# Kernel optimization log

Hardware: AMD Instinct MI355X
Metric: run time of the kernel (lower is better)

## Reference

```python
import jax, jax.numpy as jnp
import numpy as np
import math

H = 8
D_MODEL = 512
SEQ = 1024  # afr_reduced_cnn_size -> becomes sequence/channel axis
B = 16
KSIZE = 7
D_K = D_MODEL // H


def setup_inputs() -> dict:
    key = jax.random.key(0)
    ks = jax.random.split(key, 9)
    s = 0.02
    return {
        "query": jax.random.normal(ks[0], (B, SEQ, D_MODEL), jnp.float32),
        "key": jax.random.normal(ks[1], (B, SEQ, D_MODEL), jnp.float32),
        "value": jax.random.normal(ks[2], (B, SEQ, D_MODEL), jnp.float32),
        # causal conv params for K and V projections (convs[1], convs[2]); convs[0] is unused in forward
        "conv_k_w": jax.random.normal(ks[3], (SEQ, SEQ, KSIZE), jnp.float32) * s,
        "conv_k_b": jnp.zeros((SEQ,), jnp.float32),
        "conv_v_w": jax.random.normal(ks[4], (SEQ, SEQ, KSIZE), jnp.float32) * s,
        "conv_v_b": jnp.zeros((SEQ,), jnp.float32),
        # output linear (torch Linear: weight [out, in])
        "lin_w": jax.random.normal(ks[5], (D_MODEL, D_MODEL), jnp.float32) * s,
        "lin_b": jnp.zeros((D_MODEL,), jnp.float32),
    }


def _causal_conv1d(x, w, b):
    # x: [B, C, L]; w: [O, I, K]; left-pad K-1 for causality
    pad = w.shape[-1] - 1
    y = jax.lax.conv_general_dilated(
        x, w, window_strides=(1,), padding=[(pad, 0)],
        dimension_numbers=("NCH", "OIH", "NCH"))
    return y + b[None, :, None]


def reference(query, key, value, conv_k_w, conv_k_b, conv_v_w, conv_v_b, lin_w, lin_b):
    nb = query.shape[0]
    # [B, S, d_model] -> [B, h, N, d_k]
    q = query.reshape(nb, -1, H, D_K).transpose(0, 2, 1, 3)
    k = _causal_conv1d(key, conv_k_w, conv_k_b).reshape(nb, -1, H, D_K).transpose(0, 2, 1, 3)
    v = _causal_conv1d(value, conv_v_w, conv_v_b).reshape(nb, -1, H, D_K).transpose(0, 2, 1, 3)
    scores = jnp.einsum("bhnd,bhmd->bhnm", q, k) / math.sqrt(D_K)
    p_attn = jax.nn.softmax(scores, axis=-1)  # dropout is identity at eval
    x = jnp.einsum("bhnm,bhmd->bhnd", p_attn, v)
    x = x.transpose(0, 2, 1, 3).reshape(nb, -1, H * D_K)
    return x @ lin_w.T + lin_b
```

## Files before the change

### kernel.cpp

```cpp
#include <hip/hip_runtime.h>
#include <hip/hip_bf16.h>

typedef unsigned short u16;
typedef __attribute__((ext_vector_type(8))) __bf16 bf16x8;
typedef __attribute__((ext_vector_type(4))) float f32x4;
typedef __attribute__((ext_vector_type(4))) unsigned short u16x4;

#define DEVI static __device__ __forceinline__

DEVI u16 f2bf(float f) {
    union { float f; unsigned u; } v; v.f = f;
    unsigned r = v.u + 0x7fffu + ((v.u >> 16) & 1u);
    return (u16)(r >> 16);
}

DEVI unsigned cvt_pk_bf16(float lo, float hi) {
    unsigned r;
    asm("v_cvt_pk_bf16_f32 %0, %1, %2" : "=v"(r) : "v"(lo), "v"(hi));
    return r;
}

DEVI void gload16(const u16* g, u16* l) {
    __builtin_amdgcn_global_load_lds(
        (const __attribute__((address_space(1))) void*)g,
        (__attribute__((address_space(3))) void*)l, 16, 0, 0);
}


__global__ void k_cast_scale(const float* __restrict__ src, u16* __restrict__ dst,
                             int n, float scale) {
    int i = (blockIdx.x * blockDim.x + threadIdx.x) * 4;
    if (i >= n) return;
    float4 v = *(const float4*)(src + i);
    u16x4 o = { f2bf(v.x * scale), f2bf(v.y * scale), f2bf(v.z * scale), f2bf(v.w * scale) };
    *(u16x4*)(dst + i) = o;
}

__global__ void k_castW2(const float* __restrict__ wk, const float* __restrict__ wv,
                         u16* __restrict__ wtk, u16* __restrict__ wtv) {
    int oi = blockIdx.x * blockDim.x + threadIdx.x;
    const float* p = (blockIdx.y ? wv : wk) + (size_t)oi * 7;
    u16* wt = blockIdx.y ? wtv : wtk;
#pragma unroll
    for (int t = 0; t < 7; ++t)
        wt[(size_t)t * 1048576 + oi] = f2bf(p[t]);
}

__global__ void k_transpose_pad2(const float* __restrict__ xk, const float* __restrict__ xv,
                                 u16* __restrict__ ok, u16* __restrict__ ov) {
    __shared__ float tile[64][65];
    int z = blockIdx.z;
    bool isV = z >= 16;
    int b = isV ? z - 16 : z;
    const float* x = isV ? xv : xk;
    u16* out = isV ? ov : ok;
    int l0 = blockIdx.x * 64, i0 = blockIdx.y * 64;
    int t = threadIdx.x;
    const float* xb = x + (size_t)b * 1024 * 512;
    u16* ob = out + (size_t)b * 520 * 1024;
    if (blockIdx.x == 0 && t < 96) {
        int pr = t >> 4, pc = (t & 15) * 4;
        u16x4 zz = { 0, 0, 0, 0 };
        *(u16x4*)(ob + (size_t)pr * 1024 + i0 + pc) = zz;
    }
    int tr = t >> 4, tc = (t & 15) * 4;
#pragma unroll
    for (int r = 0; r < 4; ++r) {
        int row = tr + r * 16;
        float4 v = *(const float4*)(xb + (size_t)(i0 + row) * 512 + l0 + tc);
        tile[row][tc + 0] = v.x; tile[row][tc + 1] = v.y;
        tile[row][tc + 2] = v.z; tile[row][tc + 3] = v.w;
    }
    __syncthreads();
#pragma unroll
    for (int r = 0; r < 4; ++r) {
        int lr = tr + r * 16;
        u16x4 o = { f2bf(tile[tc + 0][lr]), f2bf(tile[tc + 1][lr]),
                    f2bf(tile[tc + 2][lr]), f2bf(tile[tc + 3][lr]) };
        *(u16x4*)(ob + (size_t)(l0 + 6 + lr) * 1024 + i0 + tc) = o;
    }
}

__global__ __launch_bounds__(256, 2)
void k_conv128(const u16* __restrict__ WtK, const u16* __restrict__ WtV,
               const u16* __restrict__ XtK, const u16* __restrict__ XtV,
               const float* __restrict__ bK, const float* __restrict__ bV,
               u16* __restrict__ YK, u16* __restrict__ YV) {
    __shared__ __align__(16) u16 As[2][8192];
    __shared__ __align__(16) u16 Bs[16896];
    int id = blockIdx.x;
    int o0 = (id & 7) * 128;
    bool isV = (id >> 3) & 1;
    int inner = id >> 4;
    int b = inner & 15;
    int l0 = (inner >> 4) * 256;
    const u16* Wt = isV ? WtV : WtK;
    const u16* Xb = (isV ? XtV : XtK) + (size_t)b * 520 * 1024;
    int tid = threadIdx.x, lane = tid & 63, wave = tid >> 6;
    int q = lane & 15, g = lane >> 4;
    int wm = wave >> 1, wn = wave & 1;

    int sr = tid >> 3;
    int ss = (tid & 7) ^ (sr & 7);

    auto stageA = [&](int ic, int t, int slot) {
        const u16* a = Wt + ((size_t)t << 20) + (size_t)(o0 + sr) * 1024 + (ic << 6) + ss * 8;
        u16* ad = &As[slot][tid * 8];
#pragma unroll
        for (int l = 0; l < 4; ++l)
            gload16(a + (size_t)(l << 5) * 1024, ad + (l << 11));
    };
    auto stageB = [&](int ic) {
        const u16* bb = Xb + (size_t)(l0 + sr) * 1024 + (ic << 6) + ss * 8;
        u16* bd = &Bs[tid * 8];
#pragma unroll
        for (int l = 0; l < 8; ++l)
            gload16(bb + (size_t)(l << 5) * 1024, bd + (l << 11));
        int sr5 = 256 + (sr & 7);
        gload16(Xb + (size_t)(l0 + sr5) * 1024 + (ic << 6) + ss * 8,
                &Bs[sr5 * 64 + (tid & 7) * 8]);
    };

    f32x4 acc[4][8] = {};

    stageB(0);
    stageA(0, 0, 0);
    stageA(0, 1, 1);
    asm volatile("s_waitcnt vmcnt(4)" ::: "memory");
    __builtin_amdgcn_s_barrier();

    int ic2 = 0, t2 = 2;
    for (int ic = 0; ic < 16; ++ic) {
        for (int t = 0; t < 7; ++t) {
            int s = ic * 7 + t;
            const u16* Asl = As[s & 1];
            bf16x8 af[4][2], bfr[4][2];

#pragma unroll
            for (int mf = 0; mf < 4; ++mf) {
                int r = wm * 64 + mf * 16 + q;
                const u16* base = Asl + r * 64;
#pragma unroll
                for (int kk = 0; kk < 2; ++kk)
                    af[mf][kk] = *(const bf16x8*)(base + (((kk * 4 + g) ^ (r & 7)) << 3));
            }
#pragma unroll
            for (int nf = 0; nf < 4; ++nf) {
                int r = wn * 128 + nf * 16 + q + t;
                const u16* base = Bs + r * 64;
#pragma unroll
                for (int kk = 0; kk < 2; ++kk)
                    bfr[nf][kk] = *(const bf16x8*)(base + (((kk * 4 + g) ^ (r & 7)) << 3));
            }
#pragma unroll
            for (int mf = 0; mf < 4; ++mf)
#pragma unroll
                for (int nf = 0; nf < 4; ++nf)
#pragma unroll
                    for (int kk = 0; kk < 2; ++kk)
                        acc[mf][nf] = __builtin_amdgcn_mfma_f32_16x16x32_bf16(
                            af[mf][kk], bfr[nf][kk], acc[mf][nf], 0, 0, 0);

#pragma unroll
            for (int nf = 0; nf < 4; ++nf) {
                int r = wn * 128 + (4 + nf) * 16 + q + t;
                const u16* base = Bs + r * 64;
#pragma unroll
                for (int kk = 0; kk < 2; ++kk)
                    bfr[nf][kk] = *(const bf16x8*)(base + (((kk * 4 + g) ^ (r & 7)) << 3));
            }
#pragma unroll
            for (int mf = 0; mf < 4; ++mf)
#pragma unroll
                for (int nf = 0; nf < 4; ++nf)
#pragma unroll
                    for (int kk = 0; kk < 2; ++kk)
                        acc[mf][4 + nf] = __builtin_amdgcn_mfma_f32_16x16x32_bf16(
                            af[mf][kk], bfr[nf][kk], acc[mf][4 + nf], 0, 0, 0);

            asm volatile("" ::: "memory");
            __builtin_amdgcn_s_barrier();
            if (s + 2 < 112) {
                if (t == 6) stageB(ic + 1);
                stageA(ic2, t2, s & 1);
                if (++t2 == 7) { t2 = 0; ++ic2; }
                asm volatile("s_waitcnt vmcnt(4)" ::: "memory");
            } else {
                asm volatile("s_waitcnt vmcnt(0)" ::: "memory");
            }
            __builtin_amdgcn_s_barrier();
        }
    }

    const float* bias = isV ? bV : bK;
#pragma unroll
    for (int mf = 0; mf < 4; ++mf) {
        int ro = o0 + wm * 64 + mf * 16 + g * 4;
        float b0 = bias[ro + 0], b1 = bias[ro + 1], b2 = bias[ro + 2], b3 = bias[ro + 3];
#pragma unroll
        for (int nf = 0; nf < 8; ++nf) {
            int co = l0 + wn * 128 + nf * 16 + q;
            f32x4 a = acc[mf][nf];
            if (isV) {
                u16x4 o = { f2bf(a[0] + b0), f2bf(a[1] + b1), f2bf(a[2] + b2), f2bf(a[3] + b3) };
                *(u16x4*)&YV[((size_t)b * 512 + co) * 1024 + ro] = o;
            } else {
                u16* yp = &YK[((size_t)b * 1024 + ro) * 512 + co];
                yp[0]    = f2bf(a[0] + b0);
                yp[512]  = f2bf(a[1] + b1);
                yp[1024] = f2bf(a[2] + b2);
                yp[1536] = f2bf(a[3] + b3);
            }
        }
    }
}

__global__ __launch_bounds__(512, 4)
void k_attn2(const u16* __restrict__ Q, const u16* __restrict__ K,
             const u16* __restrict__ Vt, u16* __restrict__ O) {
    __shared__ __align__(16) u16 Ks[2][64 * 64];
    __shared__ __align__(16) u16 Vs[2][64 * 64];
    int b = blockIdx.z, h = blockIdx.y, q0 = blockIdx.x * 128;
    int tid = threadIdx.x, lane = tid & 63, wave = tid >> 6;
    int g = lane >> 4, q = lane & 15;

    const u16* Kb = K + (size_t)b * 1024 * 512 + h * 64;
    const u16* Vb = Vt + ((size_t)b * 512 + h * 64) * 1024;
    const u16* Qb = Q + ((size_t)b * 1024 + q0 + wave * 16 + q) * 512 + h * 64;

    bf16x8 qf[2];
    qf[0] = *(const bf16x8*)(Qb + g * 8);
    qf[1] = *(const bf16x8*)(Qb + 32 + g * 8);

    int sr = tid >> 3;
    int ss = (tid & 7) ^ (sr & 7);
    const u16* ksrc = Kb + (size_t)sr * 512 + ss * 8;
    const u16* vsrc = Vb + (size_t)sr * 1024 + ss * 8;

    f32x4 o[4] = {};
    float lsum = 0.f;

    gload16(ksrc, &Ks[0][tid * 8]);
    gload16(vsrc, &Vs[0][tid * 8]);
    __syncthreads();

#pragma unroll 2
    for (int t = 0; t < 16; ++t) {
        int buf = t & 1;
        if (t < 15) {
            gload16(ksrc + (size_t)(t + 1) * 64 * 512, &Ks[buf ^ 1][tid * 8]);
            gload16(vsrc + (t + 1) * 64, &Vs[buf ^ 1][tid * 8]);
        }
        f32x4 s[4];
#pragma unroll
        for (int mf = 0; mf < 4; ++mf) {
            int r = 16 * mf + q;
            const u16* base = &Ks[buf][r * 64];
            bf16x8 kf0 = *(const bf16x8*)(base + (((g) ^ (q & 7)) << 3));
            bf16x8 kf1 = *(const bf16x8*)(base + (((4 + g) ^ (q & 7)) << 3));
            f32x4 zz = {};
            zz = __builtin_amdgcn_mfma_f32_16x16x32_bf16(kf0, qf[0], zz, 0, 0, 0);
            s[mf] = __builtin_amdgcn_mfma_f32_16x16x32_bf16(kf1, qf[1], zz, 0, 0, 0);
        }
        unsigned w[4][2];
#pragma unroll
        for (int mf = 0; mf < 4; ++mf) {
            f32x4 p;
#pragma unroll
            for (int j = 0; j < 4; ++j) {
                p[j] = exp2f(s[mf][j]);
                lsum += p[j];
            }
            w[mf][0] = cvt_pk_bf16(p[0], p[1]);
            w[mf][1] = cvt_pk_bf16(p[2], p[3]);
        }
        bool hi = lane >= 32;
        int ia = ((g & 1) << 5) + q;
        int ib = ia + 16;
#pragma unroll
        for (int c = 0; c < 2; ++c) {
            unsigned a0 = __shfl(w[2 * c][0], ia), b0 = __shfl(w[2 * c + 1][0], ia);
            unsigned a1 = __shfl(w[2 * c][1], ia), b1 = __shfl(w[2 * c + 1][1], ia);
            unsigned a2 = __shfl(w[2 * c][0], ib), b2 = __shfl(w[2 * c + 1][0], ib);
            unsigned a3 = __shfl(w[2 * c][1], ib), b3 = __shfl(w[2 * c + 1][1], ib);
            union { unsigned u[4]; bf16x8 v8; } pu;
            pu.u[0] = hi ? b0 : a0;
            pu.u[1] = hi ? b1 : a1;
            pu.u[2] = hi ? b2 : a2;
            pu.u[3] = hi ? b3 : a3;
            bf16x8 pb = pu.v8;
#pragma unroll
            for (int df = 0; df < 4; ++df) {
                int rd = 16 * df + q;
                bf16x8 vf = *(const bf16x8*)(&Vs[buf][rd * 64] + (((c * 4 + g) ^ (q & 7)) << 3));
                o[df] = __builtin_amdgcn_mfma_f32_16x16x32_bf16(vf, pb, o[df], 0, 0, 0);
            }
        }
        __syncthreads();
    }

    lsum += __shfl_xor(lsum, 16);
    lsum += __shfl_xor(lsum, 32);
    float inv = 1.0f / lsum;

    unsigned wo[4][2];
#pragma unroll
    for (int df = 0; df < 4; ++df) {
        f32x4 v = o[df];
        v[0] *= inv; v[1] *= inv; v[2] *= inv; v[3] *= inv;
        wo[df][0] = cvt_pk_bf16(v[0], v[1]);
        wo[df][1] = cvt_pk_bf16(v[2], v[3]);
    }
    bool hi = lane >= 32;
    int ia = ((g & 1) << 5) + q;
    int ib = ia + 16;
    u16* Ob = O + ((size_t)b * 1024 + q0 + wave * 16 + q) * 512 + h * 64;
#pragma unroll
    for (int c = 0; c < 2; ++c) {
        unsigned a0 = __shfl(wo[2 * c][0], ia), b0 = __shfl(wo[2 * c + 1][0], ia);
        unsigned a1 = __shfl(wo[2 * c][1], ia), b1 = __shfl(wo[2 * c + 1][1], ia);
        unsigned a2 = __shfl(wo[2 * c][0], ib), b2 = __shfl(wo[2 * c + 1][0], ib);
        unsigned a3 = __shfl(wo[2 * c][1], ib), b3 = __shfl(wo[2 * c + 1][1], ib);
        int4 st;
        st.x = (int)(hi ? b0 : a0);
        st.y = (int)(hi ? b1 : a1);
        st.z = (int)(hi ? b2 : a2);
        st.w = (int)(hi ? b3 : a3);
        *(int4*)(Ob + c * 32 + g * 8) = st;
    }
}

__global__ __launch_bounds__(256, 2)
void k_gemm_out(const u16* __restrict__ A, const u16* __restrict__ Bt,
                const float* __restrict__ bias, float* __restrict__ C) {
    __shared__ __align__(16) u16 As[128 * 64];
    __shared__ __align__(16) u16 Bs[128 * 64];
    int n0 = blockIdx.x * 128, m0 = blockIdx.y * 128;
    int tid = threadIdx.x, lane = tid & 63, wave = tid >> 6;
    int wr = (wave >> 1) * 64, wc = (wave & 1) * 64;
    f32x4 acc[4][4] = {};

    for (int kk = 0; kk < 8; ++kk) {
        int i0 = kk * 64;
        const u16* asrc = A + (size_t)(m0 + (tid >> 3)) * 512 + i0 + (tid & 7) * 8;
        const u16* bsrc = Bt + (size_t)(n0 + (tid >> 3)) * 512 + i0 + (tid & 7) * 8;
        __syncthreads();
#pragma unroll
        for (int s = 0; s < 4; ++s) {
            gload16(asrc + (size_t)s * 32 * 512, &As[s * 2048 + tid * 8]);
            gload16(bsrc + (size_t)s * 32 * 512, &Bs[s * 2048 + tid * 8]);
        }
        __syncthreads();
#pragma unroll
        for (int ks = 0; ks < 2; ++ks) {
            bf16x8 af[4], bfr[4];
#pragma unroll
            for (int m = 0; m < 4; ++m)
                af[m] = *(const bf16x8*)&As[(wr + m * 16 + (lane & 15)) * 64 + ks * 32 + (lane >> 4) * 8];
#pragma unroll
            for (int n = 0; n < 4; ++n)
                bfr[n] = *(const bf16x8*)&Bs[(wc + n * 16 + (lane & 15)) * 64 + ks * 32 + (lane >> 4) * 8];
#pragma unroll
            for (int m = 0; m < 4; ++m)
#pragma unroll
                for (int n = 0; n < 4; ++n)
                    acc[m][n] = __builtin_amdgcn_mfma_f32_16x16x32_bf16(af[m], bfr[n], acc[m][n], 0, 0, 0);
        }
    }

#pragma unroll
    for (int m = 0; m < 4; ++m) {
        int ro = m0 + wr + m * 16 + (lane >> 4) * 4;
#pragma unroll
        for (int n = 0; n < 4; ++n) {
            int co = n0 + wc + n * 16 + (lane & 15);
            float bb = bias[co];
            float* cp = &C[(size_t)ro * 512 + co];
            cp[0]    = acc[m][n][0] + bb;
            cp[512]  = acc[m][n][1] + bb;
            cp[1024] = acc[m][n][2] + bb;
            cp[1536] = acc[m][n][3] + bb;
        }
    }
}

extern "C" void kernel_launch(void* const* d_in, const int* in_sizes, int n_in,
                              void* d_out, int out_size, void* d_ws, size_t ws_size,
                              hipStream_t stream) {
    (void)in_sizes; (void)n_in; (void)out_size; (void)ws_size;
    const float* query = (const float*)d_in[0];
    const float* key   = (const float*)d_in[1];
    const float* value = (const float*)d_in[2];
    const float* wk    = (const float*)d_in[3];
    const float* bk    = (const float*)d_in[4];
    const float* wv    = (const float*)d_in[5];
    const float* bv    = (const float*)d_in[6];
    const float* lw    = (const float*)d_in[7];
    const float* lb    = (const float*)d_in[8];
    float* out = (float*)d_out;

    u16* ws16  = (u16*)d_ws;
    u16* q_bf  = ws16;
    u16* k_att = q_bf  + 8388608;
    u16* v_t   = k_att + 8388608;
    u16* x_att = v_t   + 8388608;
    u16* xt_k  = x_att + 8388608;
    u16* xt_v  = xt_k  + 8519680;
    u16* wk_bf = xt_v  + 8519680;
    u16* wv_bf = wk_bf + 7340032;
    u16* lw_bf = wv_bf + 7340032;

    k_cast_scale<<<8192, 256, 0, stream>>>(query, q_bf, 8388608, 0.125f * 1.44269504f);
    k_cast_scale<<<256, 256, 0, stream>>>(lw, lw_bf, 262144, 1.0f);
    k_castW2<<<dim3(4096, 2), 256, 0, stream>>>(wk, wv, wk_bf, wv_bf);
    k_transpose_pad2<<<dim3(8, 16, 32), 256, 0, stream>>>(key, value, xt_k, xt_v);

    k_conv128<<<dim3(512, 1, 1), 256, 0, stream>>>(wk_bf, wv_bf, xt_k, xt_v, bk, bv, k_att, v_t);

    k_attn2<<<dim3(8, 8, 16), 512, 0, stream>>>(q_bf, k_att, v_t, x_att);

    k_gemm_out<<<dim3(4, 128), 256, 0, stream>>>(x_att, lw_bf, lb, out);
}
```

Before: 314.4 us.

## Load conv weight fragments directly from global memory, double-buffer input tile

The convolution GEMM kernel stops staging weight tiles through LDS. Each wave now reads its A fragments straight from global memory in the layout that matches the MFMA operands. The freed LDS holds a second buffer for the input tile, so the next channel chunk is prefetched once per input-channel step rather than synchronising after every tap. This cuts the barrier count from per-tap to per-chunk, at the cost of uncoalesced 16-byte global reads of weights sitting on the MFMA critical path, with no LDS reuse across waves.

```diff
diff --git a/kernel.cpp b/kernel.cpp
--- a/kernel.cpp
+++ b/kernel.cpp
@@ -82,12 +82,11 @@
 }
 
 __global__ __launch_bounds__(256, 2)
-void k_conv128(const u16* __restrict__ WtK, const u16* __restrict__ WtV,
-               const u16* __restrict__ XtK, const u16* __restrict__ XtV,
-               const float* __restrict__ bK, const float* __restrict__ bV,
-               u16* __restrict__ YK, u16* __restrict__ YV) {
-    __shared__ __align__(16) u16 As[2][8192];
-    __shared__ __align__(16) u16 Bs[16896];
+void k_conv128g(const u16* __restrict__ WtK, const u16* __restrict__ WtV,
+                const u16* __restrict__ XtK, const u16* __restrict__ XtV,
+                const float* __restrict__ bK, const float* __restrict__ bV,
+                u16* __restrict__ YK, u16* __restrict__ YV) {
+    __shared__ __align__(16) u16 Bs[2][16896];
     int id = blockIdx.x;
     int o0 = (id & 7) * 128;
     bool isV = (id >> 3) & 1;
@@ -100,54 +99,46 @@
     int q = lane & 15, g = lane >> 4;
     int wm = wave >> 1, wn = wave & 1;
 
+    const u16* Aw = Wt + (size_t)(o0 + wm * 64 + q) * 1024 + g * 8;
+
     int sr = tid >> 3;
     int ss = (tid & 7) ^ (sr & 7);
 
-    auto stageA = [&](int ic, int t, int slot) {
-        const u16* a = Wt + ((size_t)t << 20) + (size_t)(o0 + sr) * 1024 + (ic << 6) + ss * 8;
-        u16* ad = &As[slot][tid * 8];
-#pragma unroll
-        for (int l = 0; l < 4; ++l)
-            gload16(a + (size_t)(l << 5) * 1024, ad + (l << 11));
-    };
-    auto stageB = [&](int ic) {
+    auto stageB = [&](int ic, int slot) {
         const u16* bb = Xb + (size_t)(l0 + sr) * 1024 + (ic << 6) + ss * 8;
-        u16* bd = &Bs[tid * 8];
+        u16* bd = &Bs[slot][tid * 8];
 #pragma unroll
         for (int l = 0; l < 8; ++l)
             gload16(bb + (size_t)(l << 5) * 1024, bd + (l << 11));
         int sr5 = 256 + (sr & 7);
         gload16(Xb + (size_t)(l0 + sr5) * 1024 + (ic << 6) + ss * 8,
-                &Bs[sr5 * 64 + (tid & 7) * 8]);
+                &Bs[slot][sr5 * 64 + (tid & 7) * 8]);
     };
 
     f32x4 acc[4][8] = {};
 
-    stageB(0);
-    stageA(0, 0, 0);
-    stageA(0, 1, 1);
-    asm volatile("s_waitcnt vmcnt(4)" ::: "memory");
+    stageB(0, 0);
+    asm volatile("s_waitcnt vmcnt(0)" ::: "memory");
     __builtin_amdgcn_s_barrier();
 
-    int ic2 = 0, t2 = 2;
     for (int ic = 0; ic < 16; ++ic) {
+        int slot = ic & 1;
+        if (ic + 1 < 16) stageB(ic + 1, slot ^ 1);
+        const u16* Bsl = Bs[slot];
+        const u16* Aic = Aw + (ic << 6);
+#pragma unroll
         for (int t = 0; t < 7; ++t) {
-            int s = ic * 7 + t;
-            const u16* Asl = As[s & 1];
+            const u16* At = Aic + ((size_t)t << 20);
             bf16x8 af[4][2], bfr[4][2];
-
-#pragma unroll
-            for (int mf = 0; mf < 4; ++mf) {
-                int r = wm * 64 + mf * 16 + q;
-                const u16* base = Asl + r * 64;
+#pragma unroll
+            for (int mf = 0; mf < 4; ++mf)
 #pragma unroll
                 for (int kk = 0; kk < 2; ++kk)
-                    af[mf][kk] = *(const bf16x8*)(base + (((kk * 4 + g) ^ (r & 7)) << 3));
-            }
+                    af[mf][kk] = *(const bf16x8*)(At + mf * 16384 + kk * 32);
 #pragma unroll
             for (int nf = 0; nf < 4; ++nf) {
                 int r = wn * 128 + nf * 16 + q + t;
-                const u16* base = Bs + r * 64;
+                const u16* base = Bsl + r * 64;
 #pragma unroll
                 for (int kk = 0; kk < 2; ++kk)
                     bfr[nf][kk] = *(const bf16x8*)(base + (((kk * 4 + g) ^ (r & 7)) << 3));
@@ -160,11 +151,10 @@
                     for (int kk = 0; kk < 2; ++kk)
                         acc[mf][nf] = __builtin_amdgcn_mfma_f32_16x16x32_bf16(
                             af[mf][kk], bfr[nf][kk], acc[mf][nf], 0, 0, 0);
-
 #pragma unroll
             for (int nf = 0; nf < 4; ++nf) {
                 int r = wn * 128 + (4 + nf) * 16 + q + t;
-                const u16* base = Bs + r * 64;
+                const u16* base = Bsl + r * 64;
 #pragma unroll
                 for (int kk = 0; kk < 2; ++kk)
                     bfr[nf][kk] = *(const bf16x8*)(base + (((kk * 4 + g) ^ (r & 7)) << 3));
@@ -177,19 +167,11 @@
                     for (int kk = 0; kk < 2; ++kk)
                         acc[mf][4 + nf] = __builtin_amdgcn_mfma_f32_16x16x32_bf16(
                             af[mf][kk], bfr[nf][kk], acc[mf][4 + nf], 0, 0, 0);
-
-            asm volatile("" ::: "memory");
-            __builtin_amdgcn_s_barrier();
-            if (s + 2 < 112) {
-                if (t == 6) stageB(ic + 1);
-                stageA(ic2, t2, s & 1);
-                if (++t2 == 7) { t2 = 0; ++ic2; }
-                asm volatile("s_waitcnt vmcnt(4)" ::: "memory");
-            } else {
-                asm volatile("s_waitcnt vmcnt(0)" ::: "memory");
-            }
-            __builtin_amdgcn_s_barrier();
-        }
+        }
+        asm volatile("" ::: "memory");
+        __builtin_amdgcn_s_barrier();
+        asm volatile("s_waitcnt vmcnt(0)" ::: "memory");
+        __builtin_amdgcn_s_barrier();
     }
 
     const float* bias = isV ? bV : bK;
@@ -415,7 +397,7 @@
     k_castW2<<<dim3(4096, 2), 256, 0, stream>>>(wk, wv, wk_bf, wv_bf);
     k_transpose_pad2<<<dim3(8, 16, 32), 256, 0, stream>>>(key, value, xt_k, xt_v);
 
-    k_conv128<<<dim3(512, 1, 1), 256, 0, stream>>>(wk_bf, wv_bf, xt_k, xt_v, bk, bv, k_att, v_t);
+    k_conv128g<<<dim3(512, 1, 1), 256, 0, stream>>>(wk_bf, wv_bf, xt_k, xt_v, bk, bv, k_att, v_t);
 
     k_attn2<<<dim3(8, 8, 16), 512, 0, stream>>>(q_bf, k_att, v_t, x_att);
 
```

Measured after the change: 377.3 us. 1.2x slower.
